# Kernel tuning notes

Measured on AMD Instinct MI355X. Metric: run time of the kernel, lower is better.

The kernel has to match this reference:

```python
import jax, jax.numpy as jnp
import numpy as np

NUM_HEADS = 4
LN_EPS = 1e-5
L2_EPS = 1e-12


def setup_inputs() -> dict:
    key = jax.random.key(0)
    ks = jax.random.split(key, 10)
    B, L, D, Hd = 256, 197, 768, 512
    dh = Hd // NUM_HEADS  # 128
    NC = 1000
    sc = lambda k, shape, s: jax.random.normal(k, shape, jnp.float32) * s
    return {
        "cls_token": jax.random.normal(ks[0], (B, D), jnp.float32),
        "x": jax.random.normal(ks[1], (B, L, D), jnp.float32),
        "proj_w": sc(ks[2], (D, Hd), 0.02),
        "proj_b": jnp.zeros((Hd,), jnp.float32),
        "ln_g": jnp.ones((dh,), jnp.float32),
        "ln_b": jnp.zeros((dh,), jnp.float32),
        "conv1_w": sc(ks[3], (3, 3, 3, 3), 0.2),
        "conv2_w": sc(ks[4], (3, 3, 3, 3), 0.2),
        "cls1_w": sc(ks[5], (D, NC), 0.02),
        "cls1_b": jnp.zeros((NC,), jnp.float32),
        "cls2_w": sc(ks[6], (2883, NC), 0.02),
        "cls2_b": jnp.zeros((NC,), jnp.float32),
    }


def reference(cls_token, x, proj_w, proj_b, ln_g, ln_b, conv1_w, conv2_w,
              cls1_w, cls1_b, cls2_w, cls2_b):
    B, L, D = x.shape
    dh = ln_g.shape[0]
    # proj on patch tokens (drop cls at position 0)
    xp = x[:, 1:, :] @ proj_w + proj_b            # (B, 196, 512)
    Lp = xp.shape[1]
    H = xp.shape[2] // dh
    heads = xp.reshape(B, Lp, H, dh).transpose(2, 0, 1, 3)  # (H, B, Lp, dh)
    # LayerNorm over last dim (eps=1e-5, biased var, affine)
    mu = heads.mean(-1, keepdims=True)
    var = heads.var(-1, keepdims=True)
    hn = (heads - mu) * jax.lax.rsqrt(var + LN_EPS) * ln_g + ln_b
    # Covariance._remove_mean: adaptive_avg_pool2d on (B, dh, Lp) -> mean over BOTH dh and Lp per sample
    hn = hn - hn.mean(axis=(2, 3), keepdims=True)
    # 'near' cross-covariances between adjacent heads, all pairs batched
    x1, x2 = hn[:-1], hn[1:]                      # (H-1, B, Lp, dh)
    cov = jnp.einsum('pbnd,pbne->pbde', x1, x2) / Lp  # (H-1, B, dh, dh)
    # L2 normalize over dim=2 (row axis of each dh x dh map), F.normalize eps
    nrm = jnp.sqrt(jnp.sum(cov * cov, axis=2, keepdims=True))
    cov = cov / jnp.maximum(nrm, L2_EPS)
    cov = cov.transpose(1, 0, 2, 3)               # (B, 3, 128, 128)
    conv = lambda z, w: jax.lax.conv_general_dilated(
        z, w, (2, 2), 'VALID', dimension_numbers=('NCHW', 'OIHW', 'NCHW'))
    z = conv(cov, conv1_w)                        # (B, 3, 63, 63)
    z = jax.nn.gelu(z, approximate=False)
    z = conv(z, conv2_w)                          # (B, 3, 31, 31)
    flat = z.reshape(B, -1)                       # (B, 2883)
    out = ((cls_token @ cls1_w + cls1_b) + (flat @ cls2_w + cls2_b)) / 2
    return out
```

## Files before the change

kernel.cpp:

```cpp
#include <hip/hip_runtime.h>
#include <hip/hip_bf16.h>
#include <cstdint>

typedef __bf16 bf16_t;
typedef __bf16 bf16x4 __attribute__((ext_vector_type(4)));
typedef __bf16 bf16x8 __attribute__((ext_vector_type(8)));
typedef float floatx4 __attribute__((ext_vector_type(4)));

#define LNEPS 1e-5f

__device__ inline void async_copy16(const bf16_t* g, bf16_t* l) {
    __builtin_amdgcn_global_load_lds((const __attribute__((address_space(1))) void*)g,
                                     (__attribute__((address_space(3))) void*)l,
                                     16, 0, 0);
}

__global__ __launch_bounds__(256)
void k_cvt_x(const float* __restrict__ x, bf16_t* __restrict__ xbf) {
    const int vid = blockIdx.x * 256 + threadIdx.x;
    const int row = vid / 96;
    const int kv  = vid - row * 96;
    const int b = row / 196, l = row - (row / 196) * 196;
    const float* src = x + ((b * 197 + l + 1) * 96 + kv) * 8;
    const floatx4 f0 = *(const floatx4*)src;
    const floatx4 f1 = *(const floatx4*)(src + 4);
    bf16x8 o;
#pragma unroll
    for (int e = 0; e < 4; e++) { o[e] = (bf16_t)f0[e]; o[e+4] = (bf16_t)f1[e]; }
    *(bf16x8*)(xbf + vid * 8) = o;
}

__global__ __launch_bounds__(256)
void k_transpose_w(const float* __restrict__ w, bf16_t* __restrict__ wt) {
    __shared__ bf16_t tile[32][33];
    const int bx = blockIdx.x;
    const int by = blockIdx.y;
    const int tx = threadIdx.x & 31, ty = threadIdx.x >> 5;
    for (int i = ty; i < 32; i += 8)
        tile[i][tx] = (bf16_t)w[(by*32 + i)*512 + bx*32 + tx];
    __syncthreads();
    for (int i = ty; i < 32; i += 8)
        wt[(bx*32 + i)*768 + by*32 + tx] = tile[tx][i];
}

__global__ __launch_bounds__(256, 2)
void k_proj_ln(const bf16_t* __restrict__ xbf, const bf16_t* __restrict__ wt,
               const float* __restrict__ pb, const float* __restrict__ lng,
               const float* __restrict__ lnb, bf16_t* __restrict__ hn)
{
    __shared__ bf16_t As[128*32];
    __shared__ bf16_t Bs[256*32];

    const int t = threadIdx.x;
    const int lane = t & 63;
    const int wv = t >> 6;
    const int wr = wv >> 1, wc = wv & 1;
    const int q = lane >> 4;
    const int c = lane & 15;
    const int hp = blockIdx.y;
    const int m0 = blockIdx.x * 128;

    const int srow  = t >> 2;
    const int skoff = (t & 3) * 8;
    const bf16_t* ag0 = xbf + (m0 + srow) * 768 + skoff;
    const bf16_t* ag1 = ag0 + 64*768;
    const bf16_t* bg0 = wt + (hp*256 + srow)*768 + skoff;

    floatx4 acc[4][8];
#pragma unroll
    for (int i = 0; i < 4; i++)
#pragma unroll
        for (int j = 0; j < 8; j++)
#pragma unroll
            for (int r = 0; r < 4; r++) acc[i][j][r] = 0.f;

    for (int k0 = 0; k0 < 768; k0 += 32) {
        __syncthreads();
        async_copy16(ag0 + k0, &As[t*8]);
        async_copy16(ag1 + k0, &As[2048 + t*8]);
        async_copy16(bg0 + k0,            &Bs[t*8]);
        async_copy16(bg0 + 64*768 + k0,   &Bs[2048 + t*8]);
        async_copy16(bg0 + 128*768 + k0,  &Bs[4096 + t*8]);
        async_copy16(bg0 + 192*768 + k0,  &Bs[6144 + t*8]);
        __syncthreads();
        bf16x8 af[4], bfr[8];
#pragma unroll
        for (int i = 0; i < 4; i++)
            af[i] = *(const bf16x8*)&As[(wr*64 + i*16 + c)*32 + q*8];
#pragma unroll
        for (int j = 0; j < 8; j++)
            bfr[j] = *(const bf16x8*)&Bs[(wc*128 + j*16 + c)*32 + q*8];
#pragma unroll
        for (int i = 0; i < 4; i++)
#pragma unroll
            for (int j = 0; j < 8; j++)
                acc[i][j] = __builtin_amdgcn_mfma_f32_16x16x32_bf16(af[i], bfr[j], acc[i][j], 0, 0, 0);
    }

    const int h = hp*2 + wc;
    float bias[8], gg[8], bb[8];
#pragma unroll
    for (int j = 0; j < 8; j++) {
        const int d = j*16 + c;
        bias[j] = pb[h*128 + d];
        gg[j]   = lng[d];
        bb[j]   = lnb[d];
    }
#pragma unroll
    for (int i = 0; i < 4; i++) {
#pragma unroll
        for (int r = 0; r < 4; r++) {
            float s = 0.f, s2 = 0.f;
#pragma unroll
            for (int j = 0; j < 8; j++) {
                const float v = acc[i][j][r] + bias[j];
                acc[i][j][r] = v;
                s += v; s2 += v*v;
            }
#pragma unroll
            for (int o = 1; o < 16; o <<= 1) { s += __shfl_xor(s, o); s2 += __shfl_xor(s2, o); }
            const float mu = s * (1.f/128.f);
            const float ms = s2 * (1.f/128.f);
            const float rstd = rsqrtf(ms - mu*mu + LNEPS);
            const int gm = m0 + wr*64 + i*16 + q*4 + r;
            const int bI = gm / 196, l = gm - bI*196;
            bf16_t* dst = hn + (((h*256 + bI)*196 + l) << 7);
#pragma unroll
            for (int j = 0; j < 8; j++) {
                const float v = (acc[i][j][r] - mu)*rstd*gg[j] + bb[j];
                dst[j*16 + c] = (bf16_t)v;
            }
        }
    }
}

__global__ __launch_bounds__(256)
void k_colsum(const bf16_t* __restrict__ hn, float* __restrict__ colsum)
{
    __shared__ float tmp[2][128];
    const int t = threadIdx.x;
    const int d = t & 127, half = t >> 7;
    const bf16_t* S = hn + ((long)blockIdx.x * 196 << 7);
    float s = 0.f;
    const int n0 = half * 98;
    for (int n = 0; n < 98; n++) s += (float)S[((n0 + n) << 7) + d];
    tmp[half][d] = s;
    __syncthreads();
    if (t < 128) colsum[(blockIdx.x << 7) + t] = tmp[0][t] + tmp[1][t];
}

__global__ __launch_bounds__(256, 2)
void k_cov(const bf16_t* __restrict__ hn, const float* __restrict__ colsum,
           float* __restrict__ cov)
{
    __shared__ bf16_t x1s[128*40];
    __shared__ bf16_t x2s[128*40];
    __shared__ float rs1[128], rs2[128];
    __shared__ float colsq[2][128];
    __shared__ float nrm_inv[128];
    __shared__ float mu_s[2];

    const int t = threadIdx.x;
    const int lane = t & 63;
    const int wv = t >> 6;
    const int wr = wv >> 1, wc = wv & 1;
    const int q = lane >> 4;
    const int c = lane & 15;
    const int b = blockIdx.x;
    const int p = blockIdx.y;

    const bf16_t* X1 = hn + (((p*256 + b)*196) << 7);
    const bf16_t* X2 = hn + ((((p+1)*256 + b)*196) << 7);

    if (t < 128) rs1[t] = colsum[((p*256 + b) << 7) + t];
    else         rs2[t & 127] = colsum[(((p+1)*256 + b) << 7) + (t & 127)];
    __syncthreads();
    if (wv == 0) {
        float s = rs1[lane] + rs1[lane + 64];
#pragma unroll
        for (int o = 1; o < 64; o <<= 1) s += __shfl_xor(s, o);
        if (lane == 0) mu_s[0] = s * (1.f/(196.f*128.f));
    } else if (wv == 1) {
        float s = rs2[lane] + rs2[lane + 64];
#pragma unroll
        for (int o = 1; o < 64; o <<= 1) s += __shfl_xor(s, o);
        if (lane == 0) mu_s[1] = s * (1.f/(196.f*128.f));
    }

    floatx4 acc[4][4];
#pragma unroll
    for (int i = 0; i < 4; i++)
#pragma unroll
        for (int j = 0; j < 4; j++)
#pragma unroll
            for (int r = 0; r < 4; r++) acc[i][j][r] = 0.f;

    const int nl = t >> 3;
    const int d0 = (t & 7) * 16;

    for (int n0 = 0; n0 < 224; n0 += 32) {
        __syncthreads();
        const int n = n0 + nl;
        bf16x8 va, vb, wa, wb;
        if (n < 196) {
            const bf16_t* s1 = X1 + (n << 7) + d0;
            const bf16_t* s2 = X2 + (n << 7) + d0;
            va = *(const bf16x8*)s1;
            vb = *(const bf16x8*)(s1 + 8);
            wa = *(const bf16x8*)s2;
            wb = *(const bf16x8*)(s2 + 8);
        } else {
#pragma unroll
            for (int e = 0; e < 8; e++) {
                va[e] = (bf16_t)0.f; vb[e] = (bf16_t)0.f;
                wa[e] = (bf16_t)0.f; wb[e] = (bf16_t)0.f;
            }
        }
#pragma unroll
        for (int e = 0; e < 8; e++) {
            x1s[(d0 + e)*40 + nl]     = va[e];
            x1s[(d0 + 8 + e)*40 + nl] = vb[e];
            x2s[(d0 + e)*40 + nl]     = wa[e];
            x2s[(d0 + 8 + e)*40 + nl] = wb[e];
        }
        __syncthreads();
        bf16x8 af[4], bfr[4];
#pragma unroll
        for (int i = 0; i < 4; i++)
            af[i] = *(const bf16x8*)&x1s[(wr*64 + i*16 + c)*40 + q*8];
#pragma unroll
        for (int j = 0; j < 4; j++)
            bfr[j] = *(const bf16x8*)&x2s[(wc*64 + j*16 + c)*40 + q*8];
#pragma unroll
        for (int i = 0; i < 4; i++)
#pragma unroll
            for (int j = 0; j < 4; j++)
                acc[i][j] = __builtin_amdgcn_mfma_f32_16x16x32_bf16(af[i], bfr[j], acc[i][j], 0, 0, 0);
    }

    const float mu1 = mu_s[0], mu2 = mu_s[1];
    const float invL = 1.f/196.f;
    float csq[4] = {0.f, 0.f, 0.f, 0.f};
#pragma unroll
    for (int i = 0; i < 4; i++)
#pragma unroll
        for (int j = 0; j < 4; j++)
#pragma unroll
            for (int r = 0; r < 4; r++) {
                const int d = wr*64 + i*16 + q*4 + r;
                const int e = wc*64 + j*16 + c;
                const float v = acc[i][j][r]*invL - mu2*rs1[d]*invL - mu1*rs2[e]*invL + mu1*mu2;
                acc[i][j][r] = v;
                csq[j] += v*v;
            }
#pragma unroll
    for (int j = 0; j < 4; j++) {
        float s = csq[j];
        s += __shfl_xor(s, 16);
        s += __shfl_xor(s, 32);
        csq[j] = s;
    }
    if (q == 0) {
#pragma unroll
        for (int j = 0; j < 4; j++) colsq[wr][wc*64 + j*16 + c] = csq[j];
    }
    __syncthreads();
    if (t < 128) {
        const float nr = sqrtf(colsq[0][t] + colsq[1][t]);
        nrm_inv[t] = 1.f / fmaxf(nr, 1e-12f);
    }
    __syncthreads();
    float* dst = cov + ((long)b*3 + p)*16384;
#pragma unroll
    for (int i = 0; i < 4; i++)
#pragma unroll
        for (int j = 0; j < 4; j++) {
            const int e = wc*64 + j*16 + c;
            const float ni = nrm_inv[e];
#pragma unroll
            for (int r = 0; r < 4; r++) {
                const int d = wr*64 + i*16 + q*4 + r;
                dst[(d << 7) + e] = acc[i][j][r] * ni;
            }
        }
}

__global__ __launch_bounds__(256)
void k_convs(const float* __restrict__ cov, const float* __restrict__ w1,
             const float* __restrict__ w2, bf16_t* __restrict__ Xb)
{
    __shared__ float Z[3*3969];
    __shared__ float W1s[81];
    __shared__ float W2s[81];
    const int t = threadIdx.x, b = blockIdx.x;
    if (t < 81) { W1s[t] = w1[t]; W2s[t] = w2[t]; }
    __syncthreads();
    const float* C = cov + (long)b*3*16384;
    for (int idx = t; idx < 3*3969; idx += 256) {
        const int o = idx / 3969, rem = idx - o*3969;
        const int y = rem / 63, xx = rem - y*63;
        float a = 0.f;
#pragma unroll
        for (int i = 0; i < 3; i++) {
            const float* Ci = C + i*16384 + (2*y)*128 + 2*xx;
            const float* Wi = &W1s[o*27 + i*9];
            a += Ci[0]*Wi[0]   + Ci[1]*Wi[1]   + Ci[2]*Wi[2]
               + Ci[128]*Wi[3] + Ci[129]*Wi[4] + Ci[130]*Wi[5]
               + Ci[256]*Wi[6] + Ci[257]*Wi[7] + Ci[258]*Wi[8];
        }
        Z[idx] = 0.5f*a*(1.0f + erff(a*0.70710678118654752f));
    }
    __syncthreads();
    for (int idx = t; idx < 2883; idx += 256) {
        const int o = idx / 961, rem = idx - o*961;
        const int y = rem / 31, xx = rem - y*31;
        float a = 0.f;
#pragma unroll
        for (int i = 0; i < 3; i++) {
            const float* Zi = Z + i*3969 + (2*y)*63 + 2*xx;
            const float* Wi = &W2s[(o*3+i)*9];
            a += Zi[0]*Wi[0]   + Zi[1]*Wi[1]   + Zi[2]*Wi[2]
               + Zi[63]*Wi[3]  + Zi[64]*Wi[4]  + Zi[65]*Wi[5]
               + Zi[126]*Wi[6] + Zi[127]*Wi[7] + Zi[128]*Wi[8];
        }
        Xb[(long)b*3712 + 768 + idx] = (bf16_t)a;
    }
}

__global__ __launch_bounds__(256)
void k_cvt_cls(const float* __restrict__ cls, bf16_t* __restrict__ Xb)
{
    const int t = threadIdx.x, b = blockIdx.x;
    for (int k = t; k < 768; k += 256)
        Xb[b*3712 + k] = (bf16_t)cls[b*768 + k];
    if (t < 61) Xb[b*3712 + 3651 + t] = (bf16_t)0.f;
}

__global__ __launch_bounds__(256)
void k_cvt_w(const float* __restrict__ W1, const float* __restrict__ W2,
             bf16_t* __restrict__ Wb)
{
    __shared__ bf16_t tile[32][33];
    const int k0 = blockIdx.x * 32;
    const int n0 = blockIdx.y * 32;
    const int tx = threadIdx.x & 31, ty = threadIdx.x >> 5;
    for (int i = ty; i < 32; i += 8) {
        const int k = k0 + i, n = n0 + tx;
        float v = 0.f;
        if (n < 1000 && k < 3651)
            v = (k < 768) ? W1[k*1000 + n] : W2[(k-768)*1000 + n];
        tile[i][tx] = (bf16_t)v;
    }
    __syncthreads();
    for (int i = ty; i < 32; i += 8)
        Wb[(n0 + i)*3712 + k0 + tx] = tile[tx][i];
}

__global__ __launch_bounds__(256, 2)
void k_gemm_cls(const bf16_t* __restrict__ Xb, const bf16_t* __restrict__ Wb,
                float* __restrict__ partial)
{
    __shared__ bf16_t As[128*32];
    __shared__ bf16_t Bs[128*32];

    const int t = threadIdx.x;
    const int lane = t & 63;
    const int wv = t >> 6;
    const int wr = wv >> 1, wc = wv & 1;
    const int q = lane >> 4;
    const int c = lane & 15;
    const int nt = blockIdx.x;
    const int mt = blockIdx.y;
    const int sp = blockIdx.z;

    const int srow  = t >> 2;
    const int skoff = (t & 3) * 8;
    const int m0 = mt * 128, n0 = nt * 128;
    const int kbase = sp * 928;
    const bf16_t* ag0 = Xb + (m0 + srow) * 3712 + kbase + skoff;
    const bf16_t* ag1 = Xb + (m0 + srow + 64) * 3712 + kbase + skoff;
    const bf16_t* bg0 = Wb + (n0 + srow) * 3712 + kbase + skoff;
    const bf16_t* bg1 = Wb + (n0 + srow + 64) * 3712 + kbase + skoff;

    floatx4 acc[4][4];
#pragma unroll
    for (int i = 0; i < 4; i++)
#pragma unroll
        for (int j = 0; j < 4; j++)
#pragma unroll
            for (int r = 0; r < 4; r++) acc[i][j][r] = 0.f;

    for (int k0 = 0; k0 < 928; k0 += 32) {
        __syncthreads();
        async_copy16(ag0 + k0, &As[t*8]);
        async_copy16(ag1 + k0, &As[2048 + t*8]);
        async_copy16(bg0 + k0, &Bs[t*8]);
        async_copy16(bg1 + k0, &Bs[2048 + t*8]);
        __syncthreads();
        bf16x8 af[4], bfr[4];
#pragma unroll
        for (int i = 0; i < 4; i++)
            af[i] = *(const bf16x8*)&As[(wr*64 + i*16 + c)*32 + q*8];
#pragma unroll
        for (int j = 0; j < 4; j++)
            bfr[j] = *(const bf16x8*)&Bs[(wc*64 + j*16 + c)*32 + q*8];
#pragma unroll
        for (int i = 0; i < 4; i++)
#pragma unroll
            for (int j = 0; j < 4; j++)
                acc[i][j] = __builtin_amdgcn_mfma_f32_16x16x32_bf16(af[i], bfr[j], acc[i][j], 0, 0, 0);
    }

    float* base = partial + ((long)sp*256 + m0)*1024 + n0;
#pragma unroll
    for (int i = 0; i < 4; i++)
#pragma unroll
        for (int r = 0; r < 4; r++) {
            const int row = wr*64 + i*16 + q*4 + r;
#pragma unroll
            for (int j = 0; j < 4; j++)
                base[row*1024 + wc*64 + j*16 + c] = acc[i][j][r];
        }
}

__global__ __launch_bounds__(256)
void k_cls_fin(const float* __restrict__ partial, const float* __restrict__ b1,
               const float* __restrict__ b2, float* __restrict__ out)
{
    const int idx = blockIdx.x * 256 + threadIdx.x;
    const int m = idx / 1000, n = idx - m*1000;
    float s = partial[(m)*1024 + n] + partial[(256 + m)*1024 + n]
            + partial[(512 + m)*1024 + n] + partial[(768 + m)*1024 + n];
    out[idx] = 0.5f*(s + b1[n] + b2[n]);
}

extern "C" void kernel_launch(void* const* d_in, const int* in_sizes, int n_in,
                              void* d_out, int out_size, void* d_ws, size_t ws_size,
                              hipStream_t stream) {
    const float* cls = (const float*)d_in[0];
    const float* x   = (const float*)d_in[1];
    const float* pw  = (const float*)d_in[2];
    const float* pb  = (const float*)d_in[3];
    const float* lng = (const float*)d_in[4];
    const float* lnb = (const float*)d_in[5];
    const float* c1w = (const float*)d_in[6];
    const float* c2w = (const float*)d_in[7];
    const float* w1  = (const float*)d_in[8];
    const float* b1  = (const float*)d_in[9];
    const float* w2  = (const float*)d_in[10];
    const float* b2  = (const float*)d_in[11];

    char* ws = (char*)d_ws;
    bf16_t* hn    = (bf16_t*)(ws);
    bf16_t* xbf   = (bf16_t*)(ws + 51380224ull);
    bf16_t* wt    = (bf16_t*)(ws + 128450560ull);
    float*  covb  = (float*) (ws + 51380224ull);
    float*  csum  = (float*) (ws + 129236992ull);
    bf16_t* Xb    = (bf16_t*)(ws + 129761280ull);
    bf16_t* Wb    = (bf16_t*)(ws + 131661824ull);
    float*  part  = (float*) (ws + 139264000ull);
    float*  out   = (float*)d_out;

    k_transpose_w<<<dim3(16, 24), 256, 0, stream>>>(pw, wt);
    k_cvt_x<<<18816, 256, 0, stream>>>(x, xbf);
    k_cvt_cls<<<256, 256, 0, stream>>>(cls, Xb);
    k_cvt_w<<<dim3(116, 32), 256, 0, stream>>>(w1, w2, Wb);
    k_proj_ln<<<dim3(392, 2), 256, 0, stream>>>(xbf, wt, pb, lng, lnb, hn);
    k_colsum<<<1024, 256, 0, stream>>>(hn, csum);
    k_cov<<<dim3(256, 3), 256, 0, stream>>>(hn, csum, covb);
    k_convs<<<256, 256, 0, stream>>>(covb, c1w, c2w, Xb);
    k_gemm_cls<<<dim3(8, 2, 4), 256, 0, stream>>>(Xb, Wb, part);
    k_cls_fin<<<1000, 256, 0, stream>>>(part, b1, b2, out);
}
```

Measured before the change: 433.6 us.

## Double-buffer proj GEMM with smaller tiles and vectorize colsum reads

The projection+LayerNorm GEMM now uses a 128x128 tile per block (one head) instead of 128x256, with double-buffered LDS so the next K-slice's global-to-LDS copy overlaps the MFMAs, one barrier per step, and occupancy raised to 3 blocks. The grid is reordered so the four heads sharing an M tile launch adjacently, which should help L2 reuse of the x tile. The column-sum kernel switches from scalar strided bf16 loads to 16-byte vector loads with a 16-way row split and an LDS reduction. The tradeoff is more blocks that each reload the A tile, and smaller per-warp tiles with lower MFMA-to-load ratio.

```diff
diff --git a/kernel.cpp b/kernel.cpp
--- a/kernel.cpp
+++ b/kernel.cpp
@@ -43,61 +43,66 @@
         wt[(bx*32 + i)*768 + by*32 + tx] = tile[tx][i];
 }
 
-__global__ __launch_bounds__(256, 2)
+__global__ __launch_bounds__(256, 3)
 void k_proj_ln(const bf16_t* __restrict__ xbf, const bf16_t* __restrict__ wt,
                const float* __restrict__ pb, const float* __restrict__ lng,
                const float* __restrict__ lnb, bf16_t* __restrict__ hn)
 {
-    __shared__ bf16_t As[128*32];
-    __shared__ bf16_t Bs[256*32];
+    __shared__ bf16_t As[2][128*32];
+    __shared__ bf16_t Bs[2][128*32];
 
     const int t = threadIdx.x;
     const int lane = t & 63;
     const int wv = t >> 6;
-    const int wr = wv >> 1, wc = wv & 1;
     const int q = lane >> 4;
     const int c = lane & 15;
-    const int hp = blockIdx.y;
-    const int m0 = blockIdx.x * 128;
+    const int h  = blockIdx.x;
+    const int m0 = blockIdx.y * 128;
 
     const int srow  = t >> 2;
     const int skoff = (t & 3) * 8;
-    const bf16_t* ag0 = xbf + (m0 + srow) * 768 + skoff;
-    const bf16_t* ag1 = ag0 + 64*768;
-    const bf16_t* bg0 = wt + (hp*256 + srow)*768 + skoff;
-
-    floatx4 acc[4][8];
-#pragma unroll
-    for (int i = 0; i < 4; i++)
+    const bf16_t* ag = xbf + (m0 + srow) * 768 + skoff;
+    const bf16_t* bg = wt + (h*128 + srow) * 768 + skoff;
+
+    floatx4 acc[2][8];
+#pragma unroll
+    for (int i = 0; i < 2; i++)
 #pragma unroll
         for (int j = 0; j < 8; j++)
 #pragma unroll
             for (int r = 0; r < 4; r++) acc[i][j][r] = 0.f;
 
-    for (int k0 = 0; k0 < 768; k0 += 32) {
-        __syncthreads();
-        async_copy16(ag0 + k0, &As[t*8]);
-        async_copy16(ag1 + k0, &As[2048 + t*8]);
-        async_copy16(bg0 + k0,            &Bs[t*8]);
-        async_copy16(bg0 + 64*768 + k0,   &Bs[2048 + t*8]);
-        async_copy16(bg0 + 128*768 + k0,  &Bs[4096 + t*8]);
-        async_copy16(bg0 + 192*768 + k0,  &Bs[6144 + t*8]);
-        __syncthreads();
-        bf16x8 af[4], bfr[8];
-#pragma unroll
-        for (int i = 0; i < 4; i++)
-            af[i] = *(const bf16x8*)&As[(wr*64 + i*16 + c)*32 + q*8];
+    async_copy16(ag,           &As[0][t*8]);
+    async_copy16(ag + 64*768,  &As[0][2048 + t*8]);
+    async_copy16(bg,           &Bs[0][t*8]);
+    async_copy16(bg + 64*768,  &Bs[0][2048 + t*8]);
+    __syncthreads();
+
+    int buf = 0;
+    for (int ks = 0; ks < 24; ks++) {
+        if (ks < 23) {
+            const int kn = (ks + 1) * 32;
+            async_copy16(ag + kn,           &As[buf^1][t*8]);
+            async_copy16(ag + 64*768 + kn,  &As[buf^1][2048 + t*8]);
+            async_copy16(bg + kn,           &Bs[buf^1][t*8]);
+            async_copy16(bg + 64*768 + kn,  &Bs[buf^1][2048 + t*8]);
+        }
+        bf16x8 af[2], bfr[8];
+#pragma unroll
+        for (int i = 0; i < 2; i++)
+            af[i] = *(const bf16x8*)&As[buf][(wv*32 + i*16 + c)*32 + q*8];
 #pragma unroll
         for (int j = 0; j < 8; j++)
-            bfr[j] = *(const bf16x8*)&Bs[(wc*128 + j*16 + c)*32 + q*8];
-#pragma unroll
-        for (int i = 0; i < 4; i++)
+            bfr[j] = *(const bf16x8*)&Bs[buf][(j*16 + c)*32 + q*8];
+#pragma unroll
+        for (int i = 0; i < 2; i++)
 #pragma unroll
             for (int j = 0; j < 8; j++)
                 acc[i][j] = __builtin_amdgcn_mfma_f32_16x16x32_bf16(af[i], bfr[j], acc[i][j], 0, 0, 0);
-    }
-
-    const int h = hp*2 + wc;
+        __syncthreads();
+        buf ^= 1;
+    }
+
     float bias[8], gg[8], bb[8];
 #pragma unroll
     for (int j = 0; j < 8; j++) {
@@ -107,7 +112,7 @@
         bb[j]   = lnb[d];
     }
 #pragma unroll
-    for (int i = 0; i < 4; i++) {
+    for (int i = 0; i < 2; i++) {
 #pragma unroll
         for (int r = 0; r < 4; r++) {
             float s = 0.f, s2 = 0.f;
@@ -122,7 +127,7 @@
             const float mu = s * (1.f/128.f);
             const float ms = s2 * (1.f/128.f);
             const float rstd = rsqrtf(ms - mu*mu + LNEPS);
-            const int gm = m0 + wr*64 + i*16 + q*4 + r;
+            const int gm = m0 + wv*32 + i*16 + q*4 + r;
             const int bI = gm / 196, l = gm - bI*196;
             bf16_t* dst = hn + (((h*256 + bI)*196 + l) << 7);
 #pragma unroll
@@ -137,16 +142,26 @@
 __global__ __launch_bounds__(256)
 void k_colsum(const bf16_t* __restrict__ hn, float* __restrict__ colsum)
 {
-    __shared__ float tmp[2][128];
+    __shared__ float tmp[16][128];
     const int t = threadIdx.x;
-    const int d = t & 127, half = t >> 7;
-    const bf16_t* S = hn + ((long)blockIdx.x * 196 << 7);
-    float s = 0.f;
-    const int n0 = half * 98;
-    for (int n = 0; n < 98; n++) s += (float)S[((n0 + n) << 7) + d];
-    tmp[half][d] = s;
-    __syncthreads();
-    if (t < 128) colsum[(blockIdx.x << 7) + t] = tmp[0][t] + tmp[1][t];
+    const int g = t >> 4;
+    const int dv = t & 15;
+    const bf16_t* S = hn + ((long)blockIdx.x * 196 << 7) + dv * 8;
+    float s[8] = {0.f,0.f,0.f,0.f,0.f,0.f,0.f,0.f};
+    for (int n = g; n < 196; n += 16) {
+        const bf16x8 v = *(const bf16x8*)(S + (n << 7));
+#pragma unroll
+        for (int e = 0; e < 8; e++) s[e] += (float)v[e];
+    }
+#pragma unroll
+    for (int e = 0; e < 8; e++) tmp[g][dv*8 + e] = s[e];
+    __syncthreads();
+    if (t < 128) {
+        float a = 0.f;
+#pragma unroll
+        for (int g2 = 0; g2 < 16; g2++) a += tmp[g2][t];
+        colsum[(blockIdx.x << 7) + t] = a;
+    }
 }
 
 __global__ __launch_bounds__(256, 2)
@@ -465,7 +480,7 @@
     k_cvt_x<<<18816, 256, 0, stream>>>(x, xbf);
     k_cvt_cls<<<256, 256, 0, stream>>>(cls, Xb);
     k_cvt_w<<<dim3(116, 32), 256, 0, stream>>>(w1, w2, Wb);
-    k_proj_ln<<<dim3(392, 2), 256, 0, stream>>>(xbf, wt, pb, lng, lnb, hn);
+    k_proj_ln<<<dim3(4, 392), 256, 0, stream>>>(xbf, wt, pb, lng, lnb, hn);
     k_colsum<<<1024, 256, 0, stream>>>(hn, csum);
     k_cov<<<dim3(256, 3), 256, 0, stream>>>(hn, csum, covb);
     k_convs<<<256, 256, 0, stream>>>(covb, c1w, c2w, Xb);
```

Result: no change. 439.4 us (+1.3%).
